# Kernel optimization log

Measured on AMD Instinct MI355X. Metric: run time of the kernel, lower is better.

The kernel has to match this reference:

```python
import jax, jax.numpy as jnp
import numpy as np


def setup_inputs() -> dict:
    key = jax.random.key(0)
    k1, k2, k3, k4 = jax.random.split(key, 4)
    N, E, F, H = 100000, 1600000, 128, 128
    x = jax.random.normal(k1, (N, F), dtype=jnp.float32)
    edge_index = jax.random.randint(k2, (2, E), 0, N, dtype=jnp.int64)
    W1 = jax.random.normal(k3, (F, H), dtype=jnp.float32) * (1.0 / np.sqrt(F))
    b1 = jnp.zeros((H,), dtype=jnp.float32)
    W2 = jax.random.normal(k4, (H, H), dtype=jnp.float32) * (1.0 / np.sqrt(H))
    b2 = jnp.zeros((H,), dtype=jnp.float32)
    return {"x": x, "edge_index": edge_index, "W1": W1, "b1": b1, "W2": W2, "b2": b2}


def reference(x, edge_index, W1, b1, W2, b2):
    # Two-layer cached GCN: norm is computed once (cached) and reused by both layers.
    N = x.shape[0]
    loops = jnp.arange(N, dtype=edge_index.dtype)
    src = jnp.concatenate([edge_index[0], loops])  # add self-loops
    dst = jnp.concatenate([edge_index[1], loops])
    # symmetric GCN normalization: deg^-1/2[src] * deg^-1/2[dst]
    deg = jax.ops.segment_sum(jnp.ones_like(dst, dtype=x.dtype), dst, num_segments=N)
    dinv = jnp.where(deg > 0, jax.lax.rsqrt(deg), 0.0)
    norm = dinv[src] * dinv[dst]  # [E+N]

    def conv(h, W, b):
        h = h @ W  # dense transform before sparse aggregate (cheaper: out_dim small)
        msg = norm[:, None] * h[src]  # gather + scale
        return jax.ops.segment_sum(msg, dst, num_segments=N) + b

    h = jax.nn.relu(conv(x, W1, b1))
    # dropout is identity in eval mode (deterministic reference)
    return conv(h, W2, b2)
```

## Files before the change

kernel.cpp:

```cpp
#include <hip/hip_runtime.h>


#define BKT_SHIFT 7
#define BKT_NODES 128
#define CH 8192
#define MAXBKT 1024

typedef _Float16 half4v __attribute__((ext_vector_type(4)));
typedef _Float16 half8v __attribute__((ext_vector_type(8)));
typedef float float4v __attribute__((ext_vector_type(4)));

__global__ __launch_bounds__(256) void k_bincount(const int* __restrict__ dst,
                                                  int* __restrict__ bcnt, int E, int nbkt) {
    __shared__ int sh[MAXBKT];
    for (int i = threadIdx.x; i < nbkt; i += 256) sh[i] = 0;
    __syncthreads();
    for (long long e = (long long)blockIdx.x * 256 + threadIdx.x; e < E;
         e += (long long)gridDim.x * 256)
        atomicAdd(&sh[dst[e] >> BKT_SHIFT], 1);
    __syncthreads();
    for (int i = threadIdx.x; i < nbkt; i += 256)
        if (sh[i]) atomicAdd(&bcnt[i], sh[i]);
}

__global__ __launch_bounds__(1024) void k_bscan(const int* __restrict__ bcnt,
                                                int* __restrict__ bofs,
                                                int* __restrict__ bcur, int nbkt, int E) {
    __shared__ int sh[1024];
    int t = threadIdx.x;
    int v = (t < nbkt) ? bcnt[t] : 0;
    int x = v;
    sh[t] = x;
    __syncthreads();
    for (int o = 1; o < 1024; o <<= 1) {
        int y = (t >= o) ? sh[t - o] : 0;
        __syncthreads();
        x += y;
        sh[t] = x;
        __syncthreads();
    }
    if (t < nbkt) { bofs[t] = x - v; bcur[t] = x - v; }
    if (t == 0) bofs[nbkt] = E;
}

__global__ __launch_bounds__(256) void k_binfill(const int* __restrict__ src,
                                                 const int* __restrict__ dst,
                                                 int* __restrict__ bcur,
                                                 unsigned* __restrict__ recs,
                                                 int E, int nbkt) {
    __shared__ unsigned stage[CH];
    __shared__ unsigned short stageb[CH];
    __shared__ int cnt[MAXBKT];
    __shared__ int base[MAXBKT];
    const int t = threadIdx.x;
    const long long c0 = (long long)blockIdx.x * CH;

    for (int i = t; i < nbkt; i += 256) cnt[i] = 0;
    __syncthreads();

    for (int k = 0; k < CH / 256; k++) {
        int i = k * 256 + t;
        long long e = c0 + i;
        if (e < E) {
            int d = dst[e];
            int b = d >> BKT_SHIFT;
            stage[i] = ((unsigned)(d & (BKT_NODES - 1)) << 17) | (unsigned)src[e];
            stageb[i] = (unsigned short)b;
            atomicAdd(&cnt[b], 1);
        }
    }
    __syncthreads();

    for (int i = t; i < nbkt; i += 256) {
        int c = cnt[i];
        base[i] = c ? atomicAdd(&bcur[i], c) : 0;
        cnt[i] = 0;
    }
    __syncthreads();

    for (int k = 0; k < CH / 256; k++) {
        int i = k * 256 + t;
        if (c0 + i < E) {
            int b = stageb[i];
            int p = base[b] + atomicAdd(&cnt[b], 1);
            recs[p] = stage[i];
        }
    }
}

__global__ __launch_bounds__(256) void k_deg_bins(const unsigned* __restrict__ recs,
                                                  const int* __restrict__ bofs,
                                                  int* __restrict__ deg, int n) {
    __shared__ int cnt[BKT_NODES];
    const int b = blockIdx.x, t = threadIdx.x;
    if (t < BKT_NODES) cnt[t] = 0;
    __syncthreads();
    const int beg = bofs[b], end = bofs[b + 1];
    for (int j = beg + t; j < end; j += 256)
        atomicAdd(&cnt[recs[j] >> 17], 1);
    __syncthreads();
    const int d0 = b << BKT_SHIFT;
    if (t < BKT_NODES && d0 + t < n) deg[d0 + t] = cnt[t];
}

__global__ void k_scan1(const int* __restrict__ deg, float* __restrict__ dinv,
                        int* __restrict__ ofs, int* __restrict__ sums, int n) {
    __shared__ int sh[256];
    const int t = threadIdx.x;
    const int i = blockIdx.x * 256 + t;
    int v = (i < n) ? deg[i] : 0;
    if (i < n) dinv[i] = rsqrtf((float)v + 1.0f);
    int x = v;
    sh[t] = x;
    __syncthreads();
    for (int o = 1; o < 256; o <<= 1) {
        int y = (t >= o) ? sh[t - o] : 0;
        __syncthreads();
        x += y;
        sh[t] = x;
        __syncthreads();
    }
    if (i < n) ofs[i] = x - v;
    if (t == 255) sums[blockIdx.x] = x;
}

__global__ void k_scan2(int* __restrict__ sums, int nb) {
    __shared__ int sh[512];
    const int t = threadIdx.x;
    int carry = 0;
    for (int base = 0; base < nb; base += 512) {
        int i = base + t;
        int v = (i < nb) ? sums[i] : 0;
        int x = v;
        sh[t] = x;
        __syncthreads();
        for (int o = 1; o < 512; o <<= 1) {
            int y = (t >= o) ? sh[t - o] : 0;
            __syncthreads();
            x += y;
            sh[t] = x;
            __syncthreads();
        }
        if (i < nb) sums[i] = x - v + carry;
        int tot = sh[511];
        __syncthreads();
        carry += tot;
    }
}

__global__ void k_scan3(int* __restrict__ ofs, const int* __restrict__ sums, int n, int E) {
    int i = blockIdx.x * 256 + threadIdx.x;
    if (i < n) ofs[i] += sums[blockIdx.x];
    if (i == 0) ofs[n] = E;
}

__global__ __launch_bounds__(256) void k_fill_bins(const unsigned* __restrict__ recs,
                                                   const int* __restrict__ bofs,
                                                   const int* __restrict__ ofs,
                                                   int* __restrict__ col, int n) {
    __shared__ int cur[BKT_NODES];
    const int b = blockIdx.x, t = threadIdx.x;
    const int d0 = b << BKT_SHIFT;
    if (t < BKT_NODES) cur[t] = (d0 + t < n) ? ofs[d0 + t] : 0;
    __syncthreads();
    const int beg = bofs[b], end = bofs[b + 1];
    for (int j = beg + t; j < end; j += 256) {
        unsigned r = recs[j];
        int p = atomicAdd(&cur[r >> 17], 1);
        col[p] = (int)(r & 0x1FFFF);
    }
}

__global__ __launch_bounds__(256) void k_wt(const float* __restrict__ W,
                                            _Float16* __restrict__ Wt) {
    int i = blockIdx.x * 256 + threadIdx.x;
    int k = i >> 7, c = i & 127;
    Wt[c * 128 + k] = (_Float16)W[k * 128 + c];
}

__global__ __launch_bounds__(256, 2) void k_gemm_mfma(const float* __restrict__ in,
                                                      const _Float16* __restrict__ Wt,
                                                      const float* __restrict__ dinv,
                                                      _Float16* __restrict__ out,
                                                      int n, int relu_in) {
    __shared__ _Float16 Al[64][136];
    __shared__ _Float16 Bl[128][136];
    const int t = threadIdx.x;
    const int row0 = blockIdx.x * 64;
    int nr = n - row0;
    if (nr > 64) nr = 64;

    for (int i = t; i < 128 * 16; i += 256) {
        int r = i >> 4, c8 = i & 15;
        *(half8v*)&Bl[r][c8 * 8] = *(const half8v*)&Wt[r * 128 + c8 * 8];
    }
    for (int i = t; i < nr * 32; i += 256) {
        int r = i >> 5, c4 = i & 31;
        float4 v = *(const float4*)&in[(size_t)(row0 + r) * 128 + c4 * 4];
        if (relu_in) {
            v.x = fmaxf(v.x, 0.f); v.y = fmaxf(v.y, 0.f);
            v.z = fmaxf(v.z, 0.f); v.w = fmaxf(v.w, 0.f);
        }
        half4v hv;
        hv[0] = (_Float16)v.x; hv[1] = (_Float16)v.y;
        hv[2] = (_Float16)v.z; hv[3] = (_Float16)v.w;
        *(half4v*)&Al[r][c4 * 4] = hv;
    }
    __syncthreads();

    const int wave = t >> 6;
    const int lane = t & 63;
    const int m0 = wave * 16;
    const int ml = lane & 15;
    const int quad = lane >> 4;

    float4v acc[8] = {};
#pragma unroll
    for (int kc = 0; kc < 4; kc++) {
        half8v a = *(const half8v*)&Al[m0 + ml][kc * 32 + quad * 8];
#pragma unroll
        for (int nt = 0; nt < 8; nt++) {
            half8v b = *(const half8v*)&Bl[nt * 16 + ml][kc * 32 + quad * 8];
            acc[nt] = __builtin_amdgcn_mfma_f32_16x16x32_f16(a, b, acc[nt], 0, 0, 0);
        }
    }

#pragma unroll
    for (int reg = 0; reg < 4; reg++) {
        int r = m0 + quad * 4 + reg;
        if (r < nr) {
            float dv = dinv[row0 + r];
#pragma unroll
            for (int nt = 0; nt < 8; nt++)
                out[(size_t)(row0 + r) * 128 + nt * 16 + ml] =
                    (_Float16)(acc[nt][reg] * dv);
        }
    }
}

__global__ __launch_bounds__(256) void k_agg_csr(const int* __restrict__ ofs,
                                                 const int* __restrict__ col,
                                                 const float* __restrict__ dinv,
                                                 const half4v* __restrict__ ts,
                                                 const float* __restrict__ bias,
                                                 float* __restrict__ out, int n) {
    int gid = blockIdx.x * 256 + threadIdx.x;
    int row = gid >> 5;
    int lane = gid & 31;
    if (row >= n) return;

    float dd = dinv[row];
    int beg = ofs[row];
    int end = ofs[row + 1];

    half4v sv = ts[(size_t)row * 32 + lane];
    float4 acc = make_float4((float)sv[0], (float)sv[1], (float)sv[2], (float)sv[3]);

    int j = beg;
    for (; j + 3 < end; j += 4) {
        int s0 = col[j], s1 = col[j + 1], s2 = col[j + 2], s3 = col[j + 3];
        half4v v0 = ts[(size_t)s0 * 32 + lane];
        half4v v1 = ts[(size_t)s1 * 32 + lane];
        half4v v2 = ts[(size_t)s2 * 32 + lane];
        half4v v3 = ts[(size_t)s3 * 32 + lane];
        acc.x += (float)v0[0] + (float)v1[0] + (float)v2[0] + (float)v3[0];
        acc.y += (float)v0[1] + (float)v1[1] + (float)v2[1] + (float)v3[1];
        acc.z += (float)v0[2] + (float)v1[2] + (float)v2[2] + (float)v3[2];
        acc.w += (float)v0[3] + (float)v1[3] + (float)v2[3] + (float)v3[3];
    }
    for (; j < end; j++) {
        half4v v = ts[(size_t)col[j] * 32 + lane];
        acc.x += (float)v[0];
        acc.y += (float)v[1];
        acc.z += (float)v[2];
        acc.w += (float)v[3];
    }

    float4 bv = *(const float4*)&bias[lane * 4];
    float4 o;
    o.x = bv.x + dd * acc.x;
    o.y = bv.y + dd * acc.y;
    o.z = bv.z + dd * acc.z;
    o.w = bv.w + dd * acc.w;
    *(float4*)&out[(size_t)row * 128 + lane * 4] = o;
}

extern "C" void kernel_launch(void* const* d_in, const int* in_sizes, int n_in,
                              void* d_out, int out_size, void* d_ws, size_t ws_size,
                              hipStream_t stream) {
    const int N = in_sizes[0] / 128;
    const int E = in_sizes[1] / 2;
    const float* x  = (const float*)d_in[0];
    const int*   ei = (const int*)d_in[1];
    const float* W1 = (const float*)d_in[2];
    const float* b1 = (const float*)d_in[3];
    const float* W2 = (const float*)d_in[4];
    const float* b2 = (const float*)d_in[5];

    const int* src = ei;
    const int* dst = ei + E;

    const int nb_n  = (N + 255) / 256;
    const int NBKT  = (N + BKT_NODES - 1) / BKT_NODES;

    _Float16* t    = (_Float16*)d_ws;
    _Float16* wt1  = t + (size_t)N * 128;
    _Float16* wt2  = wt1 + 16384;
    float*    dinv = (float*)(wt2 + 16384);
    int*      ofs  = (int*)(dinv + N);
    int*      deg  = ofs + N + 1;
    int*      sums = deg + N;
    unsigned* recs = (unsigned*)(sums + ((nb_n + 255) & ~255));
    int*      col  = (int*)(recs + E);
    int*      bofs = col + E;
    int*      bcur = bofs + NBKT + 1;
    int*      bcnt = bcur + NBKT;

    float* h   = (float*)d_out;
    float* out = (float*)d_out;

    const int nb_g = (N + 63) / 64;
    const int nb_a = (int)(((long long)N * 32 + 255) / 256);
    const int nb_c = (int)(((long long)E + CH - 1) / CH);

    k_wt<<<64, 256, 0, stream>>>(W1, wt1);
    k_wt<<<64, 256, 0, stream>>>(W2, wt2);
    hipMemsetAsync(bcnt, 0, (size_t)NBKT * 4, stream);
    k_bincount<<<256, 256, 0, stream>>>(dst, bcnt, E, NBKT);
    k_bscan<<<1, 1024, 0, stream>>>(bcnt, bofs, bcur, NBKT, E);
    k_binfill<<<nb_c, 256, 0, stream>>>(src, dst, bcur, recs, E, NBKT);
    k_deg_bins<<<NBKT, 256, 0, stream>>>(recs, bofs, deg, N);
    k_scan1<<<nb_n, 256, 0, stream>>>(deg, dinv, ofs, sums, N);
    k_scan2<<<1, 512, 0, stream>>>(sums, nb_n);
    k_scan3<<<nb_n, 256, 0, stream>>>(ofs, sums, N, E);
    k_fill_bins<<<NBKT, 256, 0, stream>>>(recs, bofs, ofs, col, N);

    k_gemm_mfma<<<nb_g, 256, 0, stream>>>(x, wt1, dinv, t, N, 0);
    k_agg_csr<<<nb_a, 256, 0, stream>>>(ofs, col, dinv, (const half4v*)t, b1, h, N);

    k_gemm_mfma<<<nb_g, 256, 0, stream>>>(h, wt2, dinv, t, N, 1);
    k_agg_csr<<<nb_a, 256, 0, stream>>>(ofs, col, dinv, (const half4v*)t, b2, out, N);
}
```

Measured before the change: 347.1 us.

## Store ReLU'd hidden layer in fp16, load GEMM A directly, widen aggregation lanes

The first aggregation now applies ReLU and writes the hidden activations as fp16 instead of fp32. The second GEMM reads them directly as fp16, which halves the intermediate traffic. The GEMM drops its A-tile LDS staging and loads A fragments straight from global memory, raising the occupancy hint to 4. Aggregation uses 16 lanes per row with 8-half vectors and nontemporal loads and stores. The extra fp16 rounding of the hidden layer adds some precision loss.

```diff
diff --git a/kernel.cpp b/kernel.cpp
--- a/kernel.cpp
+++ b/kernel.cpp
@@ -178,33 +178,18 @@
     Wt[c * 128 + k] = (_Float16)W[k * 128 + c];
 }
 
-__global__ __launch_bounds__(256, 2) void k_gemm_mfma(const float* __restrict__ in,
+template <int IN_HALF>
+__global__ __launch_bounds__(256, 4) void k_gemm_mfma(const void* __restrict__ inp,
                                                       const _Float16* __restrict__ Wt,
                                                       const float* __restrict__ dinv,
-                                                      _Float16* __restrict__ out,
-                                                      int n, int relu_in) {
-    __shared__ _Float16 Al[64][136];
+                                                      _Float16* __restrict__ out, int n) {
     __shared__ _Float16 Bl[128][136];
     const int t = threadIdx.x;
     const int row0 = blockIdx.x * 64;
-    int nr = n - row0;
-    if (nr > 64) nr = 64;
 
     for (int i = t; i < 128 * 16; i += 256) {
         int r = i >> 4, c8 = i & 15;
         *(half8v*)&Bl[r][c8 * 8] = *(const half8v*)&Wt[r * 128 + c8 * 8];
-    }
-    for (int i = t; i < nr * 32; i += 256) {
-        int r = i >> 5, c4 = i & 31;
-        float4 v = *(const float4*)&in[(size_t)(row0 + r) * 128 + c4 * 4];
-        if (relu_in) {
-            v.x = fmaxf(v.x, 0.f); v.y = fmaxf(v.y, 0.f);
-            v.z = fmaxf(v.z, 0.f); v.w = fmaxf(v.w, 0.f);
-        }
-        half4v hv;
-        hv[0] = (_Float16)v.x; hv[1] = (_Float16)v.y;
-        hv[2] = (_Float16)v.z; hv[3] = (_Float16)v.w;
-        *(half4v*)&Al[r][c4 * 4] = hv;
     }
     __syncthreads();
 
@@ -214,10 +199,25 @@
     const int ml = lane & 15;
     const int quad = lane >> 4;
 
+    int r = row0 + m0 + ml;
+    if (r >= n) r = n - 1;
+
     float4v acc[8] = {};
 #pragma unroll
     for (int kc = 0; kc < 4; kc++) {
-        half8v a = *(const half8v*)&Al[m0 + ml][kc * 32 + quad * 8];
+        half8v a;
+        if (IN_HALF) {
+            a = *(const half8v*)((const _Float16*)inp + (size_t)r * 128 + kc * 32 + quad * 8);
+        } else {
+            const float* ap = (const float*)inp + (size_t)r * 128 + kc * 32 + quad * 8;
+            float4v v0 = *(const float4v*)ap;
+            float4v v1 = *(const float4v*)(ap + 4);
+#pragma unroll
+            for (int k = 0; k < 4; k++) {
+                a[k] = (_Float16)v0[k];
+                a[4 + k] = (_Float16)v1[k];
+            }
+        }
 #pragma unroll
         for (int nt = 0; nt < 8; nt++) {
             half8v b = *(const half8v*)&Bl[nt * 16 + ml][kc * 32 + quad * 8];
@@ -225,64 +225,84 @@
         }
     }
 
+    int nr = n - row0;
+    if (nr > 64) nr = 64;
 #pragma unroll
     for (int reg = 0; reg < 4; reg++) {
-        int r = m0 + quad * 4 + reg;
-        if (r < nr) {
-            float dv = dinv[row0 + r];
+        int rr = m0 + quad * 4 + reg;
+        if (rr < nr) {
+            float dv = dinv[row0 + rr];
 #pragma unroll
             for (int nt = 0; nt < 8; nt++)
-                out[(size_t)(row0 + r) * 128 + nt * 16 + ml] =
+                out[(size_t)(row0 + rr) * 128 + nt * 16 + ml] =
                     (_Float16)(acc[nt][reg] * dv);
         }
     }
 }
 
+template <int OUT_HALF>
 __global__ __launch_bounds__(256) void k_agg_csr(const int* __restrict__ ofs,
                                                  const int* __restrict__ col,
                                                  const float* __restrict__ dinv,
-                                                 const half4v* __restrict__ ts,
+                                                 const half8v* __restrict__ ts,
                                                  const float* __restrict__ bias,
-                                                 float* __restrict__ out, int n) {
+                                                 void* __restrict__ outp, int n) {
     int gid = blockIdx.x * 256 + threadIdx.x;
-    int row = gid >> 5;
-    int lane = gid & 31;
+    int row = gid >> 4;
+    int lane = gid & 15;
     if (row >= n) return;
 
     float dd = dinv[row];
     int beg = ofs[row];
     int end = ofs[row + 1];
 
-    half4v sv = ts[(size_t)row * 32 + lane];
-    float4 acc = make_float4((float)sv[0], (float)sv[1], (float)sv[2], (float)sv[3]);
+    half8v sv = ts[(size_t)row * 16 + lane];
+    float acc[8];
+#pragma unroll
+    for (int k = 0; k < 8; k++) acc[k] = (float)sv[k];
 
     int j = beg;
     for (; j + 3 < end; j += 4) {
-        int s0 = col[j], s1 = col[j + 1], s2 = col[j + 2], s3 = col[j + 3];
-        half4v v0 = ts[(size_t)s0 * 32 + lane];
-        half4v v1 = ts[(size_t)s1 * 32 + lane];
-        half4v v2 = ts[(size_t)s2 * 32 + lane];
-        half4v v3 = ts[(size_t)s3 * 32 + lane];
-        acc.x += (float)v0[0] + (float)v1[0] + (float)v2[0] + (float)v3[0];
-        acc.y += (float)v0[1] + (float)v1[1] + (float)v2[1] + (float)v3[1];
-        acc.z += (float)v0[2] + (float)v1[2] + (float)v2[2] + (float)v3[2];
-        acc.w += (float)v0[3] + (float)v1[3] + (float)v2[3] + (float)v3[3];
+        int s0 = __builtin_nontemporal_load(&col[j]);
+        int s1 = __builtin_nontemporal_load(&col[j + 1]);
+        int s2 = __builtin_nontemporal_load(&col[j + 2]);
+        int s3 = __builtin_nontemporal_load(&col[j + 3]);
+        half8v v0 = ts[(size_t)s0 * 16 + lane];
+        half8v v1 = ts[(size_t)s1 * 16 + lane];
+        half8v v2 = ts[(size_t)s2 * 16 + lane];
+        half8v v3 = ts[(size_t)s3 * 16 + lane];
+#pragma unroll
+        for (int k = 0; k < 8; k++)
+            acc[k] += (float)v0[k] + (float)v1[k] + (float)v2[k] + (float)v3[k];
     }
     for (; j < end; j++) {
-        half4v v = ts[(size_t)col[j] * 32 + lane];
-        acc.x += (float)v[0];
-        acc.y += (float)v[1];
-        acc.z += (float)v[2];
-        acc.w += (float)v[3];
-    }
-
-    float4 bv = *(const float4*)&bias[lane * 4];
-    float4 o;
-    o.x = bv.x + dd * acc.x;
-    o.y = bv.y + dd * acc.y;
-    o.z = bv.z + dd * acc.z;
-    o.w = bv.w + dd * acc.w;
-    *(float4*)&out[(size_t)row * 128 + lane * 4] = o;
+        half8v v = ts[(size_t)__builtin_nontemporal_load(&col[j]) * 16 + lane];
+#pragma unroll
+        for (int k = 0; k < 8; k++) acc[k] += (float)v[k];
+    }
+
+    float4v bv0 = *(const float4v*)&bias[lane * 8];
+    float4v bv1 = *(const float4v*)&bias[lane * 8 + 4];
+
+    if (OUT_HALF) {
+        half8v hv;
+#pragma unroll
+        for (int k = 0; k < 4; k++) {
+            hv[k] = (_Float16)fmaxf(bv0[k] + dd * acc[k], 0.f);
+            hv[4 + k] = (_Float16)fmaxf(bv1[k] + dd * acc[4 + k], 0.f);
+        }
+        __builtin_nontemporal_store(hv, &((half8v*)outp)[(size_t)row * 16 + lane]);
+    } else {
+        float4v o0, o1;
+#pragma unroll
+        for (int k = 0; k < 4; k++) {
+            o0[k] = bv0[k] + dd * acc[k];
+            o1[k] = bv1[k] + dd * acc[4 + k];
+        }
+        float* op = (float*)outp + (size_t)row * 128 + lane * 8;
+        __builtin_nontemporal_store(o0, (float4v*)op);
+        __builtin_nontemporal_store(o1, (float4v*)(op + 4));
+    }
 }
 
 extern "C" void kernel_launch(void* const* d_in, const int* in_sizes, int n_in,
@@ -316,11 +336,11 @@
     int*      bcur = bofs + NBKT + 1;
     int*      bcnt = bcur + NBKT;
 
-    float* h   = (float*)d_out;
-    float* out = (float*)d_out;
+    _Float16* h16 = (_Float16*)d_out;
+    float*    out = (float*)d_out;
 
     const int nb_g = (N + 63) / 64;
-    const int nb_a = (int)(((long long)N * 32 + 255) / 256);
+    const int nb_a = (int)(((long long)N * 16 + 255) / 256);
     const int nb_c = (int)(((long long)E + CH - 1) / CH);
 
     k_wt<<<64, 256, 0, stream>>>(W1, wt1);
@@ -335,9 +355,9 @@
     k_scan3<<<nb_n, 256, 0, stream>>>(ofs, sums, N, E);
     k_fill_bins<<<NBKT, 256, 0, stream>>>(recs, bofs, ofs, col, N);
 
-    k_gemm_mfma<<<nb_g, 256, 0, stream>>>(x, wt1, dinv, t, N, 0);
-    k_agg_csr<<<nb_a, 256, 0, stream>>>(ofs, col, dinv, (const half4v*)t, b1, h, N);
-
-    k_gemm_mfma<<<nb_g, 256, 0, stream>>>(h, wt2, dinv, t, N, 1);
-    k_agg_csr<<<nb_a, 256, 0, stream>>>(ofs, col, dinv, (const half4v*)t, b2, out, N);
-}
+    k_gemm_mfma<0><<<nb_g, 256, 0, stream>>>(x, wt1, dinv, t, N);
+    k_agg_csr<1><<<nb_a, 256, 0, stream>>>(ofs, col, dinv, (const half8v*)t, b1, h16, N);
+
+    k_gemm_mfma<1><<<nb_g, 256, 0, stream>>>(h16, wt2, dinv, t, N);
+    k_agg_csr<0><<<nb_a, 256, 0, stream>>>(ofs, col, dinv, (const half8v*)t, b2, out, N);
+}
```

New measurement: 337.6 us. -2.7%, faster.

## Fuse layer-1 aggregation with layer-2 GEMM and merge scan launches

Applied to the files above, without the earlier changes.

Layer-1 aggregation now applies bias and ReLU, stages the fp16 result in LDS and immediately runs the layer-2 MFMA GEMM in the same kernel, so the fp32 hidden tensor is never written to or re-read from global memory. The small prep kernels are merged, and the bucket scan and block-sum scan are folded into their producer kernels with a last-block-done atomic counter. The first GEMM reads its A operand straight from global memory instead of through LDS, and the binfill chunk size is halved. These changes cut launches and memory traffic, but the fused kernel has a small 16-row tile, reads W2 from global per block, and the last-block pattern relies on fences for correctness.

```diff
diff --git a/kernel.cpp b/kernel.cpp
--- a/kernel.cpp
+++ b/kernel.cpp
@@ -3,43 +3,79 @@
 
 #define BKT_SHIFT 7
 #define BKT_NODES 128
-#define CH 8192
+#define CH 4096
 #define MAXBKT 1024
 
 typedef _Float16 half4v __attribute__((ext_vector_type(4)));
 typedef _Float16 half8v __attribute__((ext_vector_type(8)));
 typedef float float4v __attribute__((ext_vector_type(4)));
 
-__global__ __launch_bounds__(256) void k_bincount(const int* __restrict__ dst,
-                                                  int* __restrict__ bcnt, int E, int nbkt) {
+__global__ __launch_bounds__(256) void k_prep(const float* __restrict__ W1,
+                                              const float* __restrict__ W2,
+                                              _Float16* __restrict__ wt1,
+                                              _Float16* __restrict__ wt2,
+                                              int* __restrict__ bcnt,
+                                              int* __restrict__ dcnt, int nbkt) {
+    int i = blockIdx.x * 256 + threadIdx.x;
+    if (i < 16384) {
+        int k = i >> 7, c = i & 127;
+        wt1[c * 128 + k] = (_Float16)W1[i];
+    } else {
+        int j = i - 16384;
+        int k = j >> 7, c = j & 127;
+        wt2[c * 128 + k] = (_Float16)W2[j];
+    }
+    if (i < nbkt) bcnt[i] = 0;
+    if (i < 2) dcnt[i] = 0;
+}
+
+__global__ __launch_bounds__(256) void k_bincount_scan(const int* __restrict__ dst,
+                                                       int* __restrict__ bcnt,
+                                                       int* __restrict__ bofs,
+                                                       int* __restrict__ bcur,
+                                                       int* __restrict__ dcnt,
+                                                       int E, int nbkt, int nblocks) {
     __shared__ int sh[MAXBKT];
-    for (int i = threadIdx.x; i < nbkt; i += 256) sh[i] = 0;
-    __syncthreads();
-    for (long long e = (long long)blockIdx.x * 256 + threadIdx.x; e < E;
-         e += (long long)gridDim.x * 256)
+    const int t = threadIdx.x;
+    for (int i = t; i < nbkt; i += 256) sh[i] = 0;
+    __syncthreads();
+    for (long long e = (long long)blockIdx.x * 256 + t; e < E;
+         e += (long long)nblocks * 256)
         atomicAdd(&sh[dst[e] >> BKT_SHIFT], 1);
     __syncthreads();
-    for (int i = threadIdx.x; i < nbkt; i += 256)
+    for (int i = t; i < nbkt; i += 256)
         if (sh[i]) atomicAdd(&bcnt[i], sh[i]);
-}
-
-__global__ __launch_bounds__(1024) void k_bscan(const int* __restrict__ bcnt,
-                                                int* __restrict__ bofs,
-                                                int* __restrict__ bcur, int nbkt, int E) {
-    __shared__ int sh[1024];
-    int t = threadIdx.x;
-    int v = (t < nbkt) ? bcnt[t] : 0;
-    int x = v;
+    __threadfence();
+    __syncthreads();
+    __shared__ int last;
+    if (t == 0) last = (atomicAdd(&dcnt[0], 1) == nblocks - 1);
+    __syncthreads();
+    if (!last) return;
+    __threadfence();
+    int v[4];
+    int s = 0;
+    for (int k = 0; k < 4; k++) {
+        int idx = t * 4 + k;
+        v[k] = (idx < nbkt) ? atomicAdd(&bcnt[idx], 0) : 0;
+        s += v[k];
+    }
+    __syncthreads();
+    int x = s;
     sh[t] = x;
     __syncthreads();
-    for (int o = 1; o < 1024; o <<= 1) {
+    for (int o = 1; o < 256; o <<= 1) {
         int y = (t >= o) ? sh[t - o] : 0;
         __syncthreads();
         x += y;
         sh[t] = x;
         __syncthreads();
     }
-    if (t < nbkt) { bofs[t] = x - v; bcur[t] = x - v; }
+    int run = x - s;
+    for (int k = 0; k < 4; k++) {
+        int idx = t * 4 + k;
+        if (idx < nbkt) { bofs[idx] = run; bcur[idx] = run; }
+        run += v[k];
+    }
     if (t == 0) bofs[nbkt] = E;
 }
 
@@ -103,8 +139,12 @@
     if (t < BKT_NODES && d0 + t < n) deg[d0 + t] = cnt[t];
 }
 
-__global__ void k_scan1(const int* __restrict__ deg, float* __restrict__ dinv,
-                        int* __restrict__ ofs, int* __restrict__ sums, int n) {
+__global__ __launch_bounds__(256) void k_scan12(const int* __restrict__ deg,
+                                                float* __restrict__ dinv,
+                                                int* __restrict__ ofs,
+                                                int* __restrict__ sums,
+                                                int* __restrict__ dcnt,
+                                                int n, int nblocks) {
     __shared__ int sh[256];
     const int t = threadIdx.x;
     const int i = blockIdx.x * 256 + t;
@@ -121,30 +161,37 @@
         __syncthreads();
     }
     if (i < n) ofs[i] = x - v;
-    if (t == 255) sums[blockIdx.x] = x;
-}
-
-__global__ void k_scan2(int* __restrict__ sums, int nb) {
-    __shared__ int sh[512];
-    const int t = threadIdx.x;
-    int carry = 0;
-    for (int base = 0; base < nb; base += 512) {
-        int i = base + t;
-        int v = (i < nb) ? sums[i] : 0;
-        int x = v;
-        sh[t] = x;
-        __syncthreads();
-        for (int o = 1; o < 512; o <<= 1) {
-            int y = (t >= o) ? sh[t - o] : 0;
-            __syncthreads();
-            x += y;
-            sh[t] = x;
-            __syncthreads();
-        }
-        if (i < nb) sums[i] = x - v + carry;
-        int tot = sh[511];
-        __syncthreads();
-        carry += tot;
+    if (t == 255) atomicExch(&sums[blockIdx.x], x);
+    __threadfence();
+    __syncthreads();
+    __shared__ int last;
+    if (t == 0) last = (atomicAdd(&dcnt[1], 1) == nblocks - 1);
+    __syncthreads();
+    if (!last) return;
+    __threadfence();
+    int vv[4];
+    int s = 0;
+    for (int k = 0; k < 4; k++) {
+        int idx = t * 4 + k;
+        vv[k] = (idx < nblocks) ? atomicAdd(&sums[idx], 0) : 0;
+        s += vv[k];
+    }
+    __syncthreads();
+    int xx = s;
+    sh[t] = xx;
+    __syncthreads();
+    for (int o = 1; o < 256; o <<= 1) {
+        int y = (t >= o) ? sh[t - o] : 0;
+        __syncthreads();
+        xx += y;
+        sh[t] = xx;
+        __syncthreads();
+    }
+    int run = xx - s;
+    for (int k = 0; k < 4; k++) {
+        int idx = t * 4 + k;
+        if (idx < nblocks) sums[idx] = run;
+        run += vv[k];
     }
 }
 
@@ -171,40 +218,17 @@
     }
 }
 
-__global__ __launch_bounds__(256) void k_wt(const float* __restrict__ W,
-                                            _Float16* __restrict__ Wt) {
-    int i = blockIdx.x * 256 + threadIdx.x;
-    int k = i >> 7, c = i & 127;
-    Wt[c * 128 + k] = (_Float16)W[k * 128 + c];
-}
-
-__global__ __launch_bounds__(256, 2) void k_gemm_mfma(const float* __restrict__ in,
+__global__ __launch_bounds__(256, 4) void k_gemm_mfma(const float* __restrict__ in,
                                                       const _Float16* __restrict__ Wt,
                                                       const float* __restrict__ dinv,
-                                                      _Float16* __restrict__ out,
-                                                      int n, int relu_in) {
-    __shared__ _Float16 Al[64][136];
+                                                      _Float16* __restrict__ out, int n) {
     __shared__ _Float16 Bl[128][136];
     const int t = threadIdx.x;
     const int row0 = blockIdx.x * 64;
-    int nr = n - row0;
-    if (nr > 64) nr = 64;
 
     for (int i = t; i < 128 * 16; i += 256) {
         int r = i >> 4, c8 = i & 15;
         *(half8v*)&Bl[r][c8 * 8] = *(const half8v*)&Wt[r * 128 + c8 * 8];
-    }
-    for (int i = t; i < nr * 32; i += 256) {
-        int r = i >> 5, c4 = i & 31;
-        float4 v = *(const float4*)&in[(size_t)(row0 + r) * 128 + c4 * 4];
-        if (relu_in) {
-            v.x = fmaxf(v.x, 0.f); v.y = fmaxf(v.y, 0.f);
-            v.z = fmaxf(v.z, 0.f); v.w = fmaxf(v.w, 0.f);
-        }
-        half4v hv;
-        hv[0] = (_Float16)v.x; hv[1] = (_Float16)v.y;
-        hv[2] = (_Float16)v.z; hv[3] = (_Float16)v.w;
-        *(half4v*)&Al[r][c4 * 4] = hv;
     }
     __syncthreads();
 
@@ -214,10 +238,21 @@
     const int ml = lane & 15;
     const int quad = lane >> 4;
 
+    int r = row0 + m0 + ml;
+    if (r >= n) r = n - 1;
+
     float4v acc[8] = {};
 #pragma unroll
     for (int kc = 0; kc < 4; kc++) {
-        half8v a = *(const half8v*)&Al[m0 + ml][kc * 32 + quad * 8];
+        const float* ap = in + (size_t)r * 128 + kc * 32 + quad * 8;
+        float4v v0 = *(const float4v*)ap;
+        float4v v1 = *(const float4v*)(ap + 4);
+        half8v a;
+#pragma unroll
+        for (int k = 0; k < 4; k++) {
+            a[k] = (_Float16)v0[k];
+            a[4 + k] = (_Float16)v1[k];
+        }
 #pragma unroll
         for (int nt = 0; nt < 8; nt++) {
             half8v b = *(const half8v*)&Bl[nt * 16 + ml][kc * 32 + quad * 8];
@@ -225,25 +260,101 @@
         }
     }
 
+    int nr = n - row0;
+    if (nr > 64) nr = 64;
 #pragma unroll
     for (int reg = 0; reg < 4; reg++) {
-        int r = m0 + quad * 4 + reg;
-        if (r < nr) {
-            float dv = dinv[row0 + r];
+        int rr = m0 + quad * 4 + reg;
+        if (rr < nr) {
+            float dv = dinv[row0 + rr];
 #pragma unroll
             for (int nt = 0; nt < 8; nt++)
-                out[(size_t)(row0 + r) * 128 + nt * 16 + ml] =
+                out[(size_t)(row0 + rr) * 128 + nt * 16 + ml] =
                     (_Float16)(acc[nt][reg] * dv);
         }
     }
 }
 
-__global__ __launch_bounds__(256) void k_agg_csr(const int* __restrict__ ofs,
-                                                 const int* __restrict__ col,
-                                                 const float* __restrict__ dinv,
-                                                 const half4v* __restrict__ ts,
-                                                 const float* __restrict__ bias,
-                                                 float* __restrict__ out, int n) {
+__global__ __launch_bounds__(512, 4) void k_agg_gemm(const int* __restrict__ ofs,
+                                                     const int* __restrict__ col,
+                                                     const float* __restrict__ dinv,
+                                                     const half4v* __restrict__ ts,
+                                                     const float* __restrict__ bias,
+                                                     const _Float16* __restrict__ Wt2,
+                                                     _Float16* __restrict__ outt, int n) {
+    __shared__ __align__(16) _Float16 hl[16][136];
+    const int t = threadIdx.x;
+    const int row0 = blockIdx.x * 16;
+    const int r16 = t >> 5;
+    const int lane = t & 31;
+    const int row = row0 + r16;
+
+    float4 acc = make_float4(0.f, 0.f, 0.f, 0.f);
+    float dd = 0.f;
+    if (row < n) {
+        dd = dinv[row];
+        int beg = ofs[row];
+        int end = ofs[row + 1];
+        half4v sv = ts[(size_t)row * 32 + lane];
+        acc.x = (float)sv[0]; acc.y = (float)sv[1];
+        acc.z = (float)sv[2]; acc.w = (float)sv[3];
+        int j = beg;
+        for (; j + 3 < end; j += 4) {
+            int s0 = col[j], s1 = col[j + 1], s2 = col[j + 2], s3 = col[j + 3];
+            half4v v0 = ts[(size_t)s0 * 32 + lane];
+            half4v v1 = ts[(size_t)s1 * 32 + lane];
+            half4v v2 = ts[(size_t)s2 * 32 + lane];
+            half4v v3 = ts[(size_t)s3 * 32 + lane];
+            acc.x += (float)v0[0] + (float)v1[0] + (float)v2[0] + (float)v3[0];
+            acc.y += (float)v0[1] + (float)v1[1] + (float)v2[1] + (float)v3[1];
+            acc.z += (float)v0[2] + (float)v1[2] + (float)v2[2] + (float)v3[2];
+            acc.w += (float)v0[3] + (float)v1[3] + (float)v2[3] + (float)v3[3];
+        }
+        for (; j < end; j++) {
+            half4v v = ts[(size_t)col[j] * 32 + lane];
+            acc.x += (float)v[0];
+            acc.y += (float)v[1];
+            acc.z += (float)v[2];
+            acc.w += (float)v[3];
+        }
+    }
+    float4 bv = *(const float4*)&bias[lane * 4];
+    half4v hv;
+    hv[0] = (_Float16)fmaxf(bv.x + dd * acc.x, 0.f);
+    hv[1] = (_Float16)fmaxf(bv.y + dd * acc.y, 0.f);
+    hv[2] = (_Float16)fmaxf(bv.z + dd * acc.z, 0.f);
+    hv[3] = (_Float16)fmaxf(bv.w + dd * acc.w, 0.f);
+    *(half4v*)&hl[r16][lane * 4] = hv;
+    __syncthreads();
+
+    const int w = t >> 6;
+    const int l = t & 63;
+    const int ml = l & 15;
+    const int quad = l >> 4;
+
+    float4v acc2 = {};
+#pragma unroll
+    for (int kc = 0; kc < 4; kc++) {
+        half8v a = *(const half8v*)&hl[ml][kc * 32 + quad * 8];
+        half8v b = *(const half8v*)&Wt2[(size_t)(w * 16 + ml) * 128 + kc * 32 + quad * 8];
+        acc2 = __builtin_amdgcn_mfma_f32_16x16x32_f16(a, b, acc2, 0, 0, 0);
+    }
+#pragma unroll
+    for (int reg = 0; reg < 4; reg++) {
+        int node = row0 + quad * 4 + reg;
+        if (node < n) {
+            float dv = dinv[node];
+            outt[(size_t)node * 128 + w * 16 + ml] = (_Float16)(acc2[reg] * dv);
+        }
+    }
+}
+
+__global__ __launch_bounds__(256) void k_agg_csr32(const int* __restrict__ ofs,
+                                                   const int* __restrict__ col,
+                                                   const float* __restrict__ dinv,
+                                                   const half4v* __restrict__ ts,
+                                                   const float* __restrict__ bias,
+                                                   float* __restrict__ out, int n) {
     int gid = blockIdx.x * 256 + threadIdx.x;
     int row = gid >> 5;
     int lane = gid & 31;
@@ -315,29 +426,27 @@
     int*      bofs = col + E;
     int*      bcur = bofs + NBKT + 1;
     int*      bcnt = bcur + NBKT;
-
-    float* h   = (float*)d_out;
-    float* out = (float*)d_out;
+    int*      dcnt = bcnt + NBKT;
+
+    _Float16* ts1 = (_Float16*)d_out;
+    float*    out = (float*)d_out;
 
     const int nb_g = (N + 63) / 64;
+    const int nb_f = (N + 15) / 16;
     const int nb_a = (int)(((long long)N * 32 + 255) / 256);
     const int nb_c = (int)(((long long)E + CH - 1) / CH);
 
-    k_wt<<<64, 256, 0, stream>>>(W1, wt1);
-    k_wt<<<64, 256, 0, stream>>>(W2, wt2);
-    hipMemsetAsync(bcnt, 0, (size_t)NBKT * 4, stream);
-    k_bincount<<<256, 256, 0, stream>>>(dst, bcnt, E, NBKT);
-    k_bscan<<<1, 1024, 0, stream>>>(bcnt, bofs, bcur, NBKT, E);
+    k_prep<<<128, 256, 0, stream>>>(W1, W2, wt1, wt2, bcnt, dcnt, NBKT);
+    k_bincount_scan<<<256, 256, 0, stream>>>(dst, bcnt, bofs, bcur, dcnt, E, NBKT, 256);
     k_binfill<<<nb_c, 256, 0, stream>>>(src, dst, bcur, recs, E, NBKT);
     k_deg_bins<<<NBKT, 256, 0, stream>>>(recs, bofs, deg, N);
-    k_scan1<<<nb_n, 256, 0, stream>>>(deg, dinv, ofs, sums, N);
-    k_scan2<<<1, 512, 0, stream>>>(sums, nb_n);
+    k_scan12<<<nb_n, 256, 0, stream>>>(deg, dinv, ofs, sums, dcnt, N, nb_n);
     k_scan3<<<nb_n, 256, 0, stream>>>(ofs, sums, N, E);
     k_fill_bins<<<NBKT, 256, 0, stream>>>(recs, bofs, ofs, col, N);
 
-    k_gemm_mfma<<<nb_g, 256, 0, stream>>>(x, wt1, dinv, t, N, 0);
-    k_agg_csr<<<nb_a, 256, 0, stream>>>(ofs, col, dinv, (const half4v*)t, b1, h, N);
-
-    k_gemm_mfma<<<nb_g, 256, 0, stream>>>(h, wt2, dinv, t, N, 1);
-    k_agg_csr<<<nb_a, 256, 0, stream>>>(ofs, col, dinv, (const half4v*)t, b2, out, N);
-}
+    k_gemm_mfma<<<nb_g, 256, 0, stream>>>(x, wt1, dinv, ts1, N);
+
+    k_agg_gemm<<<nb_f, 512, 0, stream>>>(ofs, col, dinv, (const half4v*)ts1, b1, wt2, t, N);
+
+    k_agg_csr32<<<nb_a, 256, 0, stream>>>(ofs, col, dinv, (const half4v*)t, b2, out, N);
+}
```

Result: slower. 372.0 us (+7.2%).
